# Kernel optimization log

Measured on AMD Instinct MI355X. Metric: run time of the kernel, lower is better.

Reference implementation:

```python
import jax, jax.numpy as jnp
import numpy as np
import math

JULIA_ITERS = 64
ESCAPE_RADIUS = 2.0


def _julia_escape_times(seq_len, c_real, c_imag):
    # Positions mapped to the real segment [-2, 2]; iterate z <- z^2 + c,
    # record (first iteration index where |z| > R) / ITERS, else 1.0.
    x = jnp.linspace(-2.0, 2.0, seq_len)
    zr0 = x
    zi0 = jnp.zeros_like(x)
    escaped0 = jnp.zeros(seq_len, dtype=bool)
    et0 = jnp.ones(seq_len, dtype=x.dtype)
    r2 = ESCAPE_RADIUS * ESCAPE_RADIUS

    def step(carry, it):
        zr, zi, escaped, et = carry
        nzr = zr * zr - zi * zi + c_real
        nzi = 2.0 * zr * zi + c_imag
        # torch breaks out of the loop once escaped -> freeze z afterwards
        zr = jnp.where(escaped, zr, nzr)
        zi = jnp.where(escaped, zi, nzi)
        mag2 = zr * zr + zi * zi
        newly = jnp.logical_and(~escaped, mag2 > r2)
        et = jnp.where(newly, it.astype(et.dtype) / JULIA_ITERS, et)
        escaped = jnp.logical_or(escaped, newly)
        return (zr, zi, escaped, et), None

    (_, _, _, et), _ = jax.lax.scan(step, (zr0, zi0, escaped0, et0), jnp.arange(JULIA_ITERS))
    return et


def setup_inputs() -> dict:
    key = jax.random.key(0)
    kq, kk, kv = jax.random.split(key, 3)
    B, S, D = 4, 8192, 64
    return {
        "query": jax.random.normal(kq, (B, S, D), dtype=jnp.float32),
        "key": jax.random.normal(kk, (B, S, D), dtype=jnp.float32),
        "value": jax.random.normal(kv, (B, S, D), dtype=jnp.float32),
        "julia_c_real": jnp.float32(-0.7),
        "julia_c_imag": jnp.float32(0.27),
        "escape_scale": jnp.float32(1.0),
    }


def reference(query, key, value, julia_c_real, julia_c_imag, escape_scale):
    B, S, D = key.shape
    et = _julia_escape_times(S, julia_c_real, julia_c_imag)            # [S]
    julia_weights = jnp.exp(et * escape_scale)                          # [S]
    bias = jnp.log(julia_weights + 1e-8)                                # [S]
    scores = jnp.einsum("bqd,bkd->bqk", query, key) / math.sqrt(D)     # [B,S,S]
    scores = scores + bias[None, None, :]
    attn = jax.nn.softmax(scores, axis=-1)
    out = jnp.einsum("bqk,bkd->bqd", attn, value)                       # [B,S,D]
    return out  # squeeze(1) is a no-op for S > 1
```

## Files before the change

### kernel.cpp

```cpp
#include <hip/hip_runtime.h>
#include <math.h>

#define S_LEN 8192
#define DHEAD 64
#define NBATCH 4
#define BK 32
#define KIT 64

typedef unsigned short u16;
typedef unsigned int u32;
typedef __attribute__((ext_vector_type(8))) short short8;
typedef __attribute__((ext_vector_type(8))) _Float16 half8;
typedef __attribute__((ext_vector_type(2))) __fp16 fp16x2;
typedef __attribute__((ext_vector_type(4))) float f32x4;

union U16x8 { int4 i4; short8 s8; u32 w[4]; };
union HU8  { int4 i4; half8 h8; u32 w[4]; };
union H2U  { fp16x2 h2; u32 w; };
union HU   { _Float16 h; u16 u; };

#if __has_builtin(__builtin_amdgcn_exp2f)
#define EXP2(x) __builtin_amdgcn_exp2f(x)
#else
#define EXP2(x) exp2f(x)
#endif

__device__ __forceinline__ u16 f2b(float f) {
    u32 u = __float_as_uint(f);
    u32 r = (u + 0x7fffu + ((u >> 16) & 1u)) >> 16;
    return (u16)r;
}
__device__ __forceinline__ u16 f2h(float f) {
    HU x; x.h = (_Float16)f; return x.u;
}
__device__ __forceinline__ u32 packh2(float a, float b) {
    H2U x; x.h2 = __builtin_amdgcn_cvt_pkrtz(a, b); return x.w;
}

__global__ void prep_kernel(const float* __restrict__ K, const float* __restrict__ V,
                            const float* crp, const float* cip, const float* scp,
                            u16* __restrict__ blob, float* __restrict__ bias2) {
    int bid = blockIdx.x, tid = threadIdx.x;
    if (bid < 1024) {
        int b = bid >> 8, t = bid & 255;
        __shared__ float Kt[32 * 64];
        __shared__ float Vt[32 * 65];
        int row = tid >> 3, c8 = (tid & 7) * 8;
        const float* ks = K + ((size_t)(b * S_LEN + t * 32 + row)) * 64 + c8;
        const float* vs = V + ((size_t)(b * S_LEN + t * 32 + row)) * 64 + c8;
        float4 ka = *(const float4*)ks, kb4 = *(const float4*)(ks + 4);
        float4 va = *(const float4*)vs, vb4 = *(const float4*)(vs + 4);
        *(float4*)&Kt[row * 64 + c8] = ka;
        *(float4*)&Kt[row * 64 + c8 + 4] = kb4;
        float* vr = &Vt[row * 65 + c8];
        vr[0] = va.x; vr[1] = va.y; vr[2] = va.z; vr[3] = va.w;
        vr[4] = vb4.x; vr[5] = vb4.y; vr[6] = vb4.z; vr[7] = vb4.w;
        __syncthreads();

        int j = tid >> 6, lane = tid & 63, low = lane & 15, h = lane >> 4;
        u16* tb = blob + ((size_t)(b * 256 + t)) * 4096;
        {
            int kt = j >> 1, ds = j & 1;
            int krow = 8 * (low >> 2) + 4 * kt + (low & 3);
            const float* src = &Kt[krow * 64 + ds * 32 + h * 8];
            u32 wds[4];
#pragma unroll
            for (int i = 0; i < 4; ++i)
                wds[i] = (u32)f2b(src[2 * i]) | ((u32)f2b(src[2 * i + 1]) << 16);
            *(int4*)(tb + j * 512 + lane * 8) = make_int4(wds[0], wds[1], wds[2], wds[3]);
        }
        {
            int col = j * 16 + low;
            u32 wds[4];
#pragma unroll
            for (int i = 0; i < 4; ++i) {
                float a = Vt[(h * 8 + 2 * i) * 65 + col];
                float c = Vt[(h * 8 + 2 * i + 1) * 65 + col];
                wds[i] = (u32)f2h(a) | ((u32)f2h(c) << 16);
            }
            *(int4*)(tb + 2048 + j * 512 + lane * 8) = make_int4(wds[0], wds[1], wds[2], wds[3]);
        }
    } else {
#pragma clang fp contract(off)
        int i = (bid - 1024) * 256 + tid;
        double cr = (double)crp[0], ci = (double)cip[0], sc = (double)scp[0];
        double step = 4.0 / (double)(S_LEN - 1);
        double x = (i == S_LEN - 1) ? 2.0 : (-2.0 + step * (double)i);
        double zr = x, zi = 0.0, et = 1.0;
        bool esc = false;
        for (int it = 0; it < 64; ++it) {
            double nzr = zr * zr - zi * zi + cr;
            double nzi = 2.0 * zr * zi + ci;
            if (!esc) { zr = nzr; zi = nzi; }
            double m2 = zr * zr + zi * zi;
            if (!esc && m2 > 4.0) { et = (double)it / 64.0; esc = true; }
        }
        double bias = log(exp(et * sc) + 1e-8);
        bias2[i] = (float)(bias * 1.4426950408889634 - 20.0);
    }
}

__global__ __launch_bounds__(512, 4)
void flash_kernel(const float* __restrict__ Q, const u16* __restrict__ blob,
                  const float* __restrict__ bias2, float* __restrict__ Out) {
    __shared__ __align__(16) char smem[18432];

    const int tid = threadIdx.x;
    const int l = tid & 63, low = l & 15, h = l >> 4;
    const int kq = __builtin_amdgcn_readfirstlane((tid >> 6) & 3);
    const int qs = __builtin_amdgcn_readfirstlane(tid >> 8);

    const int bid = blockIdx.x;
    const int batch = bid & 3;
    const int qtile = bid >> 2;
    const int q0 = qtile * 64 + qs * 32;

    const float qscale = 0.18033688011112042f;
    short8 qfrag[2][2];
#pragma unroll
    for (int qf = 0; qf < 2; ++qf) {
        const float* qrow = Q + ((size_t)(batch * S_LEN + q0 + qf * 16 + low)) * DHEAD + h * 8;
#pragma unroll
        for (int ds = 0; ds < 2; ++ds) {
            f32x4 a = *(const f32x4*)(qrow + ds * 32);
            f32x4 b = *(const f32x4*)(qrow + ds * 32 + 4);
            U16x8 u;
#pragma unroll
            for (int jj = 0; jj < 4; ++jj) {
                u.s8[jj]     = (short)f2b(a[jj] * qscale);
                u.s8[4 + jj] = (short)f2b(b[jj] * qscale);
            }
            qfrag[qf][ds] = u.s8;
        }
    }

    const u16* kvb = blob + ((size_t)(batch * 256 + kq * 64)) * 4096;
    const int loff = l * 8;
    const float* bbase = bias2 + kq * 2048;

    f32x4 o[2][4];
#pragma unroll
    for (int qf = 0; qf < 2; ++qf)
#pragma unroll
        for (int dt = 0; dt < 4; ++dt) o[qf][dt] = (f32x4){0, 0, 0, 0};
    float lsum[2] = {0.f, 0.f};

    U16x8 kf[2][4];
    f32x4 bvv[2][2];
#pragma unroll
    for (int j = 0; j < 4; ++j) kf[0][j].i4 = *(const int4*)(kvb + j * 512 + loff);
    bvv[0][0] = *(const f32x4*)(bbase + h * 8);
    bvv[0][1] = *(const f32x4*)(bbase + h * 8 + 4);

#pragma unroll 2
    for (int ki = 0; ki < KIT; ++ki) {
        const int c = ki & 1;
        const u16* tb = kvb + ki * 4096;

        HU8 vf[4];
#pragma unroll
        for (int j = 0; j < 4; ++j) vf[j].i4 = *(const int4*)(tb + 2048 + j * 512 + loff);

        const u16* tn = tb + 4096;
#pragma unroll
        for (int j = 0; j < 4; ++j) kf[c ^ 1][j].i4 = *(const int4*)(tn + j * 512 + loff);
        const float* bpn = bbase + (ki + 1) * 32 + h * 8;
        bvv[c ^ 1][0] = *(const f32x4*)bpn;
        bvv[c ^ 1][1] = *(const f32x4*)(bpn + 4);

        HU8 pf[2];
#pragma unroll
        for (int kt = 0; kt < 2; ++kt) {
            const f32x4 binit = kt ? bvv[c][1] : bvv[c][0];
            f32x4 st[2];
#pragma unroll
            for (int qf = 0; qf < 2; ++qf) {
                f32x4 a = __builtin_amdgcn_mfma_f32_16x16x32_bf16(kf[c][kt * 2].s8, qfrag[qf][0], binit, 0, 0, 0);
                a = __builtin_amdgcn_mfma_f32_16x16x32_bf16(kf[c][kt * 2 + 1].s8, qfrag[qf][1], a, 0, 0, 0);
                st[qf] = a;
            }
#pragma unroll
            for (int qf = 0; qf < 2; ++qf) {
                float p0 = EXP2(st[qf][0]), p1 = EXP2(st[qf][1]);
                float p2 = EXP2(st[qf][2]), p3 = EXP2(st[qf][3]);
                lsum[qf] += (p0 + p1) + (p2 + p3);
                pf[qf].w[kt * 2]     = packh2(p0, p1);
                pf[qf].w[kt * 2 + 1] = packh2(p2, p3);
            }
        }

#pragma unroll
        for (int dt = 0; dt < 4; ++dt)
#pragma unroll
            for (int qf = 0; qf < 2; ++qf)
                o[qf][dt] = __builtin_amdgcn_mfma_f32_16x16x32_f16(vf[dt].h8, pf[qf].h8, o[qf][dt], 0, 0, 0);
    }

#pragma unroll
    for (int qf = 0; qf < 2; ++qf) {
        lsum[qf] += __shfl_xor(lsum[qf], 16, 64);
        lsum[qf] += __shfl_xor(lsum[qf], 32, 64);
    }

    float* MO = (float*)smem;
    float* ML = (float*)(smem + 17408);
    const int baserow = qs * 32 + low;
#pragma unroll 1
    for (int src = 1; src < 4; ++src) {
        __syncthreads();
        if (kq == src) {
#pragma unroll
            for (int qf = 0; qf < 2; ++qf) {
                const int row = baserow + qf * 16;
#pragma unroll
                for (int dt = 0; dt < 4; ++dt)
                    *(f32x4*)&MO[row * 68 + dt * 16 + h * 4] = o[qf][dt];
                if (h == 0) ML[row] = lsum[qf];
            }
        }
        __syncthreads();
        if (kq == 0) {
#pragma unroll
            for (int qf = 0; qf < 2; ++qf) {
                const int row = baserow + qf * 16;
#pragma unroll
                for (int dt = 0; dt < 4; ++dt) {
                    f32x4 a = *(const f32x4*)&MO[row * 68 + dt * 16 + h * 4];
#pragma unroll
                    for (int jj = 0; jj < 4; ++jj) o[qf][dt][jj] += a[jj];
                }
                lsum[qf] += ML[row];
            }
        }
    }

    if (kq == 0) {
#pragma unroll
        for (int qf = 0; qf < 2; ++qf) {
            const float inv = 1.f / lsum[qf];
            float* orow = Out + ((size_t)(batch * S_LEN + qtile * 64 + qs * 32 + qf * 16 + low)) * DHEAD;
#pragma unroll
            for (int dt = 0; dt < 4; ++dt) {
                f32x4 r;
#pragma unroll
                for (int jj = 0; jj < 4; ++jj) r[jj] = o[qf][dt][jj] * inv;
                *(f32x4*)(orow + dt * 16 + h * 4) = r;
            }
        }
    }
}

extern "C" void kernel_launch(void* const* d_in, const int* in_sizes, int n_in,
                              void* d_out, int out_size, void* d_ws, size_t ws_size,
                              hipStream_t stream) {
    const float* Q  = (const float*)d_in[0];
    const float* K  = (const float*)d_in[1];
    const float* V  = (const float*)d_in[2];
    const float* cr = (const float*)d_in[3];
    const float* ci = (const float*)d_in[4];
    const float* sc = (const float*)d_in[5];
    float* out = (float*)d_out;

    char* ws = (char*)d_ws;
    float* bias2 = (float*)ws;
    u16*   blob  = (u16*)(ws + 32768);

    prep_kernel<<<dim3(1056), dim3(256), 0, stream>>>(K, V, cr, ci, sc, blob, bias2);
    flash_kernel<<<dim3(512), dim3(512), 0, stream>>>(Q, blob, bias2, out);
}
```

Baseline: 171.7 us.

## Give each wave 64 query rows per K/V load and switch QK to fp16

The flash kernel block shrinks from 512 to 256 threads. Each wave now covers all 64 query rows (four 16-row fragments) against its quarter of the key range, so every K/V fragment loaded from global memory feeds twice as many MFMAs. Q and K are converted to fp16 instead of bf16, which lets the QK product use the f16 MFMA. In exchange, register pressure rises (o grows to 4x4 accumulators) and occupancy may drop, and fp16 narrows the representable range of the scaled scores.

```diff
diff --git a/kernel.cpp b/kernel.cpp
--- a/kernel.cpp
+++ b/kernel.cpp
@@ -9,15 +9,13 @@
 
 typedef unsigned short u16;
 typedef unsigned int u32;
-typedef __attribute__((ext_vector_type(8))) short short8;
 typedef __attribute__((ext_vector_type(8))) _Float16 half8;
 typedef __attribute__((ext_vector_type(2))) __fp16 fp16x2;
 typedef __attribute__((ext_vector_type(4))) float f32x4;
 
-union U16x8 { int4 i4; short8 s8; u32 w[4]; };
-union HU8  { int4 i4; half8 h8; u32 w[4]; };
-union H2U  { fp16x2 h2; u32 w; };
-union HU   { _Float16 h; u16 u; };
+union HU8 { int4 i4; half8 h8; u32 w[4]; };
+union H2U { fp16x2 h2; u32 w; };
+union HU  { _Float16 h; u16 u; };
 
 #if __has_builtin(__builtin_amdgcn_exp2f)
 #define EXP2(x) __builtin_amdgcn_exp2f(x)
@@ -25,11 +23,6 @@
 #define EXP2(x) exp2f(x)
 #endif
 
-__device__ __forceinline__ u16 f2b(float f) {
-    u32 u = __float_as_uint(f);
-    u32 r = (u + 0x7fffu + ((u >> 16) & 1u)) >> 16;
-    return (u16)r;
-}
 __device__ __forceinline__ u16 f2h(float f) {
     HU x; x.h = (_Float16)f; return x.u;
 }
@@ -66,7 +59,7 @@
             u32 wds[4];
 #pragma unroll
             for (int i = 0; i < 4; ++i)
-                wds[i] = (u32)f2b(src[2 * i]) | ((u32)f2b(src[2 * i + 1]) << 16);
+                wds[i] = (u32)f2h(src[2 * i]) | ((u32)f2h(src[2 * i + 1]) << 16);
             *(int4*)(tb + j * 512 + lane * 8) = make_int4(wds[0], wds[1], wds[2], wds[3]);
         }
         {
@@ -100,37 +93,35 @@
     }
 }
 
-__global__ __launch_bounds__(512, 4)
+__global__ __launch_bounds__(256, 2)
 void flash_kernel(const float* __restrict__ Q, const u16* __restrict__ blob,
                   const float* __restrict__ bias2, float* __restrict__ Out) {
-    __shared__ __align__(16) char smem[18432];
+    __shared__ __align__(16) char smem[17664];
 
     const int tid = threadIdx.x;
     const int l = tid & 63, low = l & 15, h = l >> 4;
-    const int kq = __builtin_amdgcn_readfirstlane((tid >> 6) & 3);
-    const int qs = __builtin_amdgcn_readfirstlane(tid >> 8);
+    const int kq = __builtin_amdgcn_readfirstlane(tid >> 6);
 
     const int bid = blockIdx.x;
     const int batch = bid & 3;
     const int qtile = bid >> 2;
-    const int q0 = qtile * 64 + qs * 32;
+    const int q0 = qtile * 64;
 
     const float qscale = 0.18033688011112042f;
-    short8 qfrag[2][2];
-#pragma unroll
-    for (int qf = 0; qf < 2; ++qf) {
+    half8 qfrag[4][2];
+#pragma unroll
+    for (int qf = 0; qf < 4; ++qf) {
         const float* qrow = Q + ((size_t)(batch * S_LEN + q0 + qf * 16 + low)) * DHEAD + h * 8;
 #pragma unroll
         for (int ds = 0; ds < 2; ++ds) {
             f32x4 a = *(const f32x4*)(qrow + ds * 32);
             f32x4 b = *(const f32x4*)(qrow + ds * 32 + 4);
-            U16x8 u;
-#pragma unroll
-            for (int jj = 0; jj < 4; ++jj) {
-                u.s8[jj]     = (short)f2b(a[jj] * qscale);
-                u.s8[4 + jj] = (short)f2b(b[jj] * qscale);
-            }
-            qfrag[qf][ds] = u.s8;
+            HU8 u;
+            u.w[0] = packh2(a[0] * qscale, a[1] * qscale);
+            u.w[1] = packh2(a[2] * qscale, a[3] * qscale);
+            u.w[2] = packh2(b[0] * qscale, b[1] * qscale);
+            u.w[3] = packh2(b[2] * qscale, b[3] * qscale);
+            qfrag[qf][ds] = u.h8;
         }
     }
 
@@ -138,14 +129,14 @@
     const int loff = l * 8;
     const float* bbase = bias2 + kq * 2048;
 
-    f32x4 o[2][4];
-#pragma unroll
-    for (int qf = 0; qf < 2; ++qf)
+    f32x4 o[4][4];
+#pragma unroll
+    for (int qf = 0; qf < 4; ++qf)
 #pragma unroll
         for (int dt = 0; dt < 4; ++dt) o[qf][dt] = (f32x4){0, 0, 0, 0};
-    float lsum[2] = {0.f, 0.f};
-
-    U16x8 kf[2][4];
+    float lsum[4] = {0.f, 0.f, 0.f, 0.f};
+
+    HU8 kf[2][4];
     f32x4 bvv[2][2];
 #pragma unroll
     for (int j = 0; j < 4; ++j) kf[0][j].i4 = *(const int4*)(kvb + j * 512 + loff);
@@ -168,19 +159,19 @@
         bvv[c ^ 1][0] = *(const f32x4*)bpn;
         bvv[c ^ 1][1] = *(const f32x4*)(bpn + 4);
 
-        HU8 pf[2];
+        HU8 pf[4];
 #pragma unroll
         for (int kt = 0; kt < 2; ++kt) {
             const f32x4 binit = kt ? bvv[c][1] : bvv[c][0];
-            f32x4 st[2];
-#pragma unroll
-            for (int qf = 0; qf < 2; ++qf) {
-                f32x4 a = __builtin_amdgcn_mfma_f32_16x16x32_bf16(kf[c][kt * 2].s8, qfrag[qf][0], binit, 0, 0, 0);
-                a = __builtin_amdgcn_mfma_f32_16x16x32_bf16(kf[c][kt * 2 + 1].s8, qfrag[qf][1], a, 0, 0, 0);
+            f32x4 st[4];
+#pragma unroll
+            for (int qf = 0; qf < 4; ++qf) {
+                f32x4 a = __builtin_amdgcn_mfma_f32_16x16x32_f16(kf[c][kt * 2].h8, qfrag[qf][0], binit, 0, 0, 0);
+                a = __builtin_amdgcn_mfma_f32_16x16x32_f16(kf[c][kt * 2 + 1].h8, qfrag[qf][1], a, 0, 0, 0);
                 st[qf] = a;
             }
 #pragma unroll
-            for (int qf = 0; qf < 2; ++qf) {
+            for (int qf = 0; qf < 4; ++qf) {
                 float p0 = EXP2(st[qf][0]), p1 = EXP2(st[qf][1]);
                 float p2 = EXP2(st[qf][2]), p3 = EXP2(st[qf][3]);
                 lsum[qf] += (p0 + p1) + (p2 + p3);
@@ -192,26 +183,25 @@
 #pragma unroll
         for (int dt = 0; dt < 4; ++dt)
 #pragma unroll
-            for (int qf = 0; qf < 2; ++qf)
+            for (int qf = 0; qf < 4; ++qf)
                 o[qf][dt] = __builtin_amdgcn_mfma_f32_16x16x32_f16(vf[dt].h8, pf[qf].h8, o[qf][dt], 0, 0, 0);
     }
 
 #pragma unroll
-    for (int qf = 0; qf < 2; ++qf) {
+    for (int qf = 0; qf < 4; ++qf) {
         lsum[qf] += __shfl_xor(lsum[qf], 16, 64);
         lsum[qf] += __shfl_xor(lsum[qf], 32, 64);
     }
 
     float* MO = (float*)smem;
     float* ML = (float*)(smem + 17408);
-    const int baserow = qs * 32 + low;
 #pragma unroll 1
     for (int src = 1; src < 4; ++src) {
         __syncthreads();
         if (kq == src) {
 #pragma unroll
-            for (int qf = 0; qf < 2; ++qf) {
-                const int row = baserow + qf * 16;
+            for (int qf = 0; qf < 4; ++qf) {
+                const int row = qf * 16 + low;
 #pragma unroll
                 for (int dt = 0; dt < 4; ++dt)
                     *(f32x4*)&MO[row * 68 + dt * 16 + h * 4] = o[qf][dt];
@@ -221,8 +211,8 @@
         __syncthreads();
         if (kq == 0) {
 #pragma unroll
-            for (int qf = 0; qf < 2; ++qf) {
-                const int row = baserow + qf * 16;
+            for (int qf = 0; qf < 4; ++qf) {
+                const int row = qf * 16 + low;
 #pragma unroll
                 for (int dt = 0; dt < 4; ++dt) {
                     f32x4 a = *(const f32x4*)&MO[row * 68 + dt * 16 + h * 4];
@@ -236,9 +226,9 @@
 
     if (kq == 0) {
 #pragma unroll
-        for (int qf = 0; qf < 2; ++qf) {
+        for (int qf = 0; qf < 4; ++qf) {
             const float inv = 1.f / lsum[qf];
-            float* orow = Out + ((size_t)(batch * S_LEN + qtile * 64 + qs * 32 + qf * 16 + low)) * DHEAD;
+            float* orow = Out + ((size_t)(batch * S_LEN + q0 + qf * 16 + low)) * DHEAD;
 #pragma unroll
             for (int dt = 0; dt < 4; ++dt) {
                 f32x4 r;
@@ -266,5 +256,5 @@
     u16*   blob  = (u16*)(ws + 32768);
 
     prep_kernel<<<dim3(1056), dim3(256), 0, stream>>>(K, V, cr, ci, sc, blob, bias2);
-    flash_kernel<<<dim3(512), dim3(512), 0, stream>>>(Q, blob, bias2, out);
-}
+    flash_kernel<<<dim3(512), dim3(256), 0, stream>>>(Q, blob, bias2, out);
+}
```

New measurement: 149.7 us. 12.8% less time.
